# Performance work log

Hardware: AMD Instinct MI355X
Metric: run time of the kernel (lower is better)

Reference implementation:

```python
import jax, jax.numpy as jnp
import numpy as np

V, E, H2, B, T, OUT = 50000, 300, 512, 32, 512, 256
H = H2 // 2  # hidden per direction


def _rand_mask(key, lengths, n_true):
    # exactly n_true True positions per row, all within the valid prefix [0, len)
    t = jnp.arange(T)[None, :]
    r = jax.random.uniform(key, (B, T)) + (t >= lengths[:, None]) * 10.0
    idx = jnp.argsort(r, axis=1)[:, :n_true]
    mask = jnp.zeros((B, T), dtype=bool)
    return mask.at[jnp.arange(B)[:, None], idx].set(True)


def setup_inputs() -> dict:
    key = jax.random.key(0)
    ks = jax.random.split(key, 12)
    inputs = jax.random.randint(ks[0], (B, T), 0, V)
    lengths = jnp.sort(jax.random.randint(ks[1], (B,), OUT, T + 1))[::-1]
    lengths = lengths.at[0].set(T)  # max length == padded length
    fmask = _rand_mask(ks[2], lengths, OUT)
    bmask = _rand_mask(ks[3], lengths, OUT)
    emb_scale = np.sqrt(3.0 / E).astype(np.float32)
    emb = jax.random.uniform(ks[4], (V, E), minval=-emb_scale, maxval=emb_scale, dtype=jnp.float32)
    k = 1.0 / np.sqrt(H).astype(np.float32)
    def u(kk, shape):
        return jax.random.uniform(kk, shape, minval=-k, maxval=k, dtype=jnp.float32)
    return {
        'inputs': inputs, 'seq_length': lengths, 'fmask': fmask, 'bmask': bmask,
        'out_seq_length': OUT, 'emb': emb,
        'W_ih_f': u(ks[5], (4 * H, E)), 'W_hh_f': u(ks[6], (4 * H, H)),
        'b_ih_f': u(ks[7], (4 * H,)), 'b_hh_f': u(ks[8], (4 * H,)),
        'W_ih_b': u(ks[9], (4 * H, E)), 'W_hh_b': u(ks[10], (4 * H, H)),
        'b_ih_b': u(ks[11], (4 * H,)), 'b_hh_b': u(ks[7], (4 * H,)),
    }


def run_lstm(xe, W_ih, W_hh, b_ih, b_hh):
    # PyTorch LSTM cell, gate order i,f,g,o. xe: (B,T,E) -> (B,T,H)
    xg = jnp.einsum('bte,ge->btg', xe, W_ih) + (b_ih + b_hh)
    def step(carry, xg_t):
        h, c = carry
        g = xg_t + h @ W_hh.T
        i, f, gg, o = jnp.split(g, 4, axis=-1)
        c = jax.nn.sigmoid(f) * c + jax.nn.sigmoid(i) * jnp.tanh(gg)
        h = jax.nn.sigmoid(o) * jnp.tanh(c)
        return (h, c), h
    h0 = jnp.zeros((xe.shape[0], W_hh.shape[1]), xe.dtype)
    _, hs = jax.lax.scan(step, (h0, h0), xg.transpose(1, 0, 2))
    return hs.transpose(1, 0, 2)


def select_masked(x, mask, out_len):
    # masked_select row-major order == indices of True in increasing t
    idx = jnp.argsort(jnp.logical_not(mask), axis=1, stable=True)[:, :out_len]
    return jnp.take_along_axis(x, idx[:, :, None], axis=1)


def reference(inputs, seq_length, fmask, bmask, out_seq_length, emb,
              W_ih_f, W_hh_f, b_ih_f, b_hh_f, W_ih_b, W_hh_b, b_ih_b, b_hh_b):
    t = jnp.arange(inputs.shape[1])[None, :]          # (1,T)
    valid = t < seq_length[:, None]                   # (B,T)
    # forward direction (dropout is identity at inference)
    f_out = run_lstm(emb[inputs], W_ih_f, W_hh_f, b_ih_f, b_hh_f)
    f_out = f_out * valid[..., None]                  # pad_packed zeros beyond len
    fsel = select_masked(f_out, fmask, out_seq_length)
    # per-batch sequence reversal of valid prefix (padding stays in place)
    rev_idx = jnp.where(valid, seq_length[:, None] - 1 - t, t)
    rinputs = jnp.take_along_axis(inputs, rev_idx, axis=1)
    b_out = run_lstm(emb[rinputs], W_ih_b, W_hh_b, b_ih_b, b_hh_b)
    b_out = b_out * valid[..., None]
    bsel = select_masked(b_out, bmask, out_seq_length)
    # re-reverse selected backward outputs per batch
    k = jnp.minimum(seq_length, out_seq_length)[:, None]
    t2 = jnp.arange(out_seq_length)[None, :]
    idx2 = jnp.where(t2 < k, out_seq_length - 1 - t2, t2 - k)
    bsel = jnp.take_along_axis(bsel, idx2[:, :, None], axis=1)
    return jnp.concatenate([fsel, bsel], axis=2)      # (B,out_seq,2H)
```

## Files before the change

kernel.cpp:

```cpp
#include <hip/hip_runtime.h>
#include <hip/hip_bf16.h>

#define B_   32
#define T_   512
#define E_   300
#define H_   256
#define OUT_ 256
#define ECH  100
#define GROWP 293

typedef unsigned long long u64;

__global__ __launch_bounds__(64) void slots_kernel(
    const unsigned char* __restrict__ fm, const unsigned char* __restrict__ bm,
    int* __restrict__ fslot, int* __restrict__ bpos)
{
    __shared__ unsigned char fL[B_ * T_];
    __shared__ unsigned char bL[B_ * T_];
    const int tid = threadIdx.x;

    const unsigned int* fw = (const unsigned int*)fm;
    int cnt = 0;
    for (int i = tid; i < 128; i += 64) {
        unsigned int v = fw[i];
        cnt += ((v & 0xFFu) != 0) + ((v & 0xFF00u) != 0)
             + ((v & 0xFF0000u) != 0) + ((v >> 24) != 0);
    }
#pragma unroll
    for (int off = 32; off; off >>= 1) cnt += __shfl_down(cnt, off, 64);
    bool isbool = __shfl(cnt, 0, 64) > 128;

    if (isbool) {
        for (int i = tid; i < B_ * T_ / 4; i += 64) {
            ((unsigned int*)fL)[i] = ((const unsigned int*)fm)[i];
            ((unsigned int*)bL)[i] = ((const unsigned int*)bm)[i];
        }
    } else {
        const unsigned int* bw = (const unsigned int*)bm;
        for (int i = tid; i < B_ * T_; i += 64) {
            fL[i] = fw[i] != 0;
            bL[i] = bw[i] != 0;
        }
    }
    __syncthreads();

    if (tid < B_) {
        int jf = 0, jb = 0;
        for (int t = 0; t < T_; ++t) {
            bool f = fL[tid * T_ + t] != 0;
            bool g = bL[tid * T_ + t] != 0;
            fslot[tid * T_ + t] = f ? (jf++) : -1;
            bpos [tid * T_ + t] = g ? (OUT_ - 1 - (jb++)) : -1;
        }
    }
}

__global__ __launch_bounds__(256) void xg_gemm(
    const int* __restrict__ inputs, const int* __restrict__ seqlen,
    const float* __restrict__ emb,
    const float* __restrict__ Wihf, const float* __restrict__ Wihb,
    const float* __restrict__ bihf, const float* __restrict__ bhhf,
    const float* __restrict__ bihb, const float* __restrict__ bhhb,
    float* __restrict__ xg, int t0, int TcMax)
{
    const int tg   = blockIdx.y;
    const int dir  = blockIdx.z;
    const int rblk = blockIdx.x * 64;
    const int tid  = threadIdx.x;

    __shared__ float eL[4][B_][ECH];
    __shared__ int   tokS[4][B_];

    if (tid < 128) {
        int t4 = tid >> 5, b = tid & 31;
        int t = t0 + tg * 4 + t4;
        int L = seqlen[b];
        int tt = t;
        if (dir) tt = (t < L) ? (L - 1 - t) : t;
        tokS[t4][b] = inputs[b * T_ + tt];
    }

    const float* W = dir ? Wihb : Wihf;
    const int b  = tid & 31;
    const int r8 = tid >> 5;

    float acc[4][8];
#pragma unroll
    for (int t4 = 0; t4 < 4; ++t4)
#pragma unroll
        for (int m = 0; m < 8; ++m) acc[t4][m] = 0.f;

    for (int ec = 0; ec < 3; ++ec) {
        __syncthreads();
        for (int idx = tid; idx < 3200; idx += 256) {
            int q  = idx % 25;
            int bb = (idx / 25) & 31;
            int t4 = idx / (25 * 32);
            const float* erow = emb + (size_t)tokS[t4][bb] * E_ + ec * ECH;
            *(float4*)&eL[t4][bb][q * 4] = *(const float4*)(erow + q * 4);
        }
        __syncthreads();

        for (int e4 = 0; e4 < 25; ++e4) {
            float4 w4[8];
#pragma unroll
            for (int m = 0; m < 8; ++m)
                w4[m] = *(const float4*)(W + (size_t)(rblk + r8 + m * 8) * E_
                                         + ec * ECH + e4 * 4);
#pragma unroll
            for (int t4 = 0; t4 < 4; ++t4) {
                float4 h4 = *(const float4*)&eL[t4][b][e4 * 4];
#pragma unroll
                for (int m = 0; m < 8; ++m)
                    acc[t4][m] += h4.x * w4[m].x + h4.y * w4[m].y
                                + h4.z * w4[m].z + h4.w * w4[m].w;
            }
        }
    }

    const float* bi = dir ? bihb : bihf;
    const float* bh = dir ? bhhb : bhhf;
#pragma unroll
    for (int t4 = 0; t4 < 4; ++t4) {
        float* outp = xg + (size_t)(dir * TcMax + tg * 4 + t4) * (1024 * B_);
#pragma unroll
        for (int m = 0; m < 8; ++m) {
            int row = rblk + r8 + m * 8;
            outp[(size_t)row * B_ + b] = acc[t4][m] + bi[row] + bh[row];
        }
    }
}

__global__ __launch_bounds__(512, 2) void persist_rec(
    const float* __restrict__ xg, const int* __restrict__ seqlen,
    const float* __restrict__ Whh_f, const float* __restrict__ Whh_b,
    const int* __restrict__ fslot, const int* __restrict__ bpos,
    float* __restrict__ hbuf, float* __restrict__ cbuf,
    int* __restrict__ barr, float* __restrict__ out, int t0, int Tc)
{
    const int wg  = blockIdx.x;
    const int dir = wg >> 6;
    const int wgd = wg & 63;
    const int u0  = wgd * 4;
    const int tid = threadIdx.x;

    const int rg  = tid & 3;
    const int bgr = (tid >> 2) & 7;
    const int kq  = tid >> 5;

    __shared__ float hP[128 * 68];
    __shared__ float gbuf[16 * GROWP];
    __shared__ int   sL[B_];

    const float* Whh = dir ? Whh_b : Whh_f;
    float w[4][16];
#pragma unroll
    for (int r = 0; r < 4; ++r) {
        const float* wr = Whh + (size_t)(rg * H_ + u0 + r) * H_ + kq * 16;
#pragma unroll
        for (int q = 0; q < 4; ++q) {
            float4 v = *(const float4*)(wr + q * 4);
            w[r][q * 4 + 0] = v.x; w[r][q * 4 + 1] = v.y;
            w[r][q * 4 + 2] = v.z; w[r][q * 4 + 3] = v.w;
        }
    }
    if (tid < B_) sL[tid] = seqlen[tid];
    __syncthreads();

    const int ul = (tid >> 5) & 3, bb = tid & 31;
    float c_reg = 0.f;
    if (t0 > 0 && tid < 128)
        c_reg = cbuf[(size_t)(dir * 64 + wgd) * 128 + ul * 32 + bb];

    float xgv0 = 0.f, xgv1 = 0.f, xgv2 = 0.f, xgv3 = 0.f;
    if (tid < 128) {
        const float* xp = xg + (size_t)(dir * Tc) * 32768 + (u0 + ul) * 32 + bb;
        xgv0 = xp[0];
        xgv1 = xp[256 * 32];
        xgv2 = xp[512 * 32];
        xgv3 = xp[768 * 32];
    }

    int* myflag = barr + dir * 64 + wgd;

    for (int tc = 0; tc < Tc; ++tc) {
        const int t = t0 + tc;

        float xgn0 = 0.f, xgn1 = 0.f, xgn2 = 0.f, xgn3 = 0.f;
        if (tc + 1 < Tc && tid < 128) {
            const float* xp = xg + (size_t)(dir * Tc + tc + 1) * 32768 + (u0 + ul) * 32 + bb;
            xgn0 = xp[0];
            xgn1 = xp[256 * 32];
            xgn2 = xp[512 * 32];
            xgn3 = xp[768 * 32];
        }

        if (tc > 0) {
            if (tid < 64) {
                const int* fp = barr + dir * 64 + tid;
                while (!__all(__hip_atomic_load(fp, __ATOMIC_RELAXED,
                                                __HIP_MEMORY_SCOPE_AGENT) >= tc))
                    __builtin_amdgcn_s_sleep(1);
            }
            __syncthreads();
        }

        u64 hr[8];
        if (t > 0) {
            const u64* hp64 = (const u64*)(hbuf +
                (size_t)(dir * 2 + ((t - 1) & 1)) * (64 * 32 * 4));
#pragma unroll
            for (int i = 0; i < 8; ++i)
                hr[i] = __hip_atomic_load(hp64 + tid + 512 * i, __ATOMIC_RELAXED,
                                          __HIP_MEMORY_SCOPE_AGENT);
#pragma unroll
            for (int i = 0; i < 8; ++i) {
                int g = tid + 512 * i;
                int f4 = g >> 1, jp = g & 1;
                int k4 = f4 >> 5, b = f4 & 31;
                int base = ((k4 >> 2) * 8 + (b >> 2)) * 68 + (k4 & 3) * 16 + (b & 3);
                union { u64 u; float f[2]; } cv; cv.u = hr[i];
                hP[base + 8 * jp]     = cv.f[0];
                hP[base + 8 * jp + 4] = cv.f[1];
            }
        }
        __syncthreads();

        float acc[4][4];
#pragma unroll
        for (int r = 0; r < 4; ++r)
#pragma unroll
            for (int bi = 0; bi < 4; ++bi) acc[r][bi] = 0.f;

        if (t > 0) {
            const float* hblk = &hP[(kq * 8 + bgr) * 68];
#pragma unroll
            for (int kk = 0; kk < 16; ++kk) {
                float4 h4 = *(const float4*)(hblk + kk * 4);
#pragma unroll
                for (int r = 0; r < 4; ++r) {
                    acc[r][0] += w[r][kk] * h4.x;
                    acc[r][1] += w[r][kk] * h4.y;
                    acc[r][2] += w[r][kk] * h4.z;
                    acc[r][3] += w[r][kk] * h4.w;
                }
            }
        }

#pragma unroll
        for (int r = 0; r < 4; ++r)
#pragma unroll
            for (int bi = 0; bi < 4; ++bi)
                acc[r][bi] += __shfl_xor(acc[r][bi], 32, 64);

        if (((tid >> 5) & 1) == 0) {
            const int kq2 = kq >> 1;
#pragma unroll
            for (int r = 0; r < 4; ++r)
#pragma unroll
                for (int bi = 0; bi < 4; ++bi)
                    gbuf[(r * 4 + rg) * GROWP + (bgr * 4 + bi) * 9 + kq2] = acc[r][bi];
        }
        __syncthreads();

        if (tid < 128) {
            const int u = u0 + ul;
            float hnew;
            if (t < sL[bb]) {
                float gi = xgv0, gf = xgv1, gg = xgv2, go = xgv3;
#pragma unroll
                for (int q = 0; q < 8; ++q) {
                    gi += gbuf[(ul * 4 + 0) * GROWP + bb * 9 + q];
                    gf += gbuf[(ul * 4 + 1) * GROWP + bb * 9 + q];
                    gg += gbuf[(ul * 4 + 2) * GROWP + bb * 9 + q];
                    go += gbuf[(ul * 4 + 3) * GROWP + bb * 9 + q];
                }
                float si = 1.f / (1.f + expf(-gi));
                float sf = 1.f / (1.f + expf(-gf));
                float so = 1.f / (1.f + expf(-go));
                c_reg = sf * c_reg + si * tanhf(gg);
                hnew  = so * tanhf(c_reg);
                if (dir == 0) {
                    int j = fslot[bb * T_ + t];
                    if (j >= 0)
                        __hip_atomic_store(&out[((size_t)bb * OUT_ + j) * 512 + u],
                                           hnew, __ATOMIC_RELAXED,
                                           __HIP_MEMORY_SCOPE_AGENT);
                } else {
                    int p = bpos[bb * T_ + t];
                    if (p >= 0)
                        __hip_atomic_store(&out[((size_t)bb * OUT_ + p) * 512 + 256 + u],
                                           hnew, __ATOMIC_RELAXED,
                                           __HIP_MEMORY_SCOPE_AGENT);
                }
            } else {
                hnew = hP[((u >> 4) * 8 + (bb >> 2)) * 68 + (u & 15) * 4 + (bb & 3)];
            }
            float* hn = hbuf + (size_t)(dir * 2 + (t & 1)) * (64 * 32 * 4);
            __hip_atomic_store(&hn[(wgd * 32 + bb) * 4 + ul], hnew,
                               __ATOMIC_RELAXED, __HIP_MEMORY_SCOPE_AGENT);
        }
        xgv0 = xgn0; xgv1 = xgn1; xgv2 = xgn2; xgv3 = xgn3;
        __syncthreads();

        if (tc + 1 < Tc && tid == 0)
            __hip_atomic_store(myflag, tc + 1, __ATOMIC_RELAXED,
                               __HIP_MEMORY_SCOPE_AGENT);
    }

    if (tid < 128)
        cbuf[(size_t)(dir * 64 + wgd) * 128 + ul * 32 + bb] = c_reg;
}

extern "C" void kernel_launch(void* const* d_in, const int* in_sizes, int n_in,
                              void* d_out, int out_size, void* d_ws, size_t ws_size,
                              hipStream_t stream) {
    const int*           inputs = (const int*)d_in[0];
    const int*           seqlen = (const int*)d_in[1];
    const unsigned char* fm     = (const unsigned char*)d_in[2];
    const unsigned char* bm     = (const unsigned char*)d_in[3];
    const float* emb  = (const float*)d_in[5];
    const float* Wihf = (const float*)d_in[6];
    const float* Whhf = (const float*)d_in[7];
    const float* bihf = (const float*)d_in[8];
    const float* bhhf = (const float*)d_in[9];
    const float* Wihb = (const float*)d_in[10];
    const float* Whhb = (const float*)d_in[11];
    const float* bihb = (const float*)d_in[12];
    const float* bhhb = (const float*)d_in[13];
    float* out = (float*)d_out;

    char* ws = (char*)d_ws;
    int*   fslot = (int*)(ws);
    int*   bpos  = (int*)(ws + 65536);
    float* hbuf  = (float*)(ws + 131072);
    float* cbuf  = (float*)(ws + 262144);
    int*   barr  = (int*)(ws + 327680);
    float* xg    = (float*)(ws + 393216);
    (void)in_sizes; (void)n_in; (void)out_size;

    size_t avail = (ws_size > 393216) ? ws_size - 393216 : 0;
    int Tc = 4;
    for (int c = 512; c >= 4; c >>= 1)
        if ((size_t)c * 262144 <= avail) { Tc = c; break; }

    slots_kernel<<<1, 64, 0, stream>>>(fm, bm, fslot, bpos);

    for (int t0 = 0; t0 < T_; t0 += Tc) {
        dim3 g(16, Tc / 4, 2);
        xg_gemm<<<g, 256, 0, stream>>>(inputs, seqlen, emb, Wihf, Wihb,
                                       bihf, bhhf, bihb, bhhb, xg, t0, Tc);
        hipMemsetAsync(barr, 0, 512, stream);
        persist_rec<<<128, 512, 0, stream>>>(xg, seqlen, Whhf, Whhb,
                                             fslot, bpos, hbuf, cbuf, barr, out, t0, Tc);
    }
}
```

Baseline: 2.324 ms.

## Fuse input-projection GEMM into persistent LSTM kernel with producer-consumer flags

Merges the input projection GEMM and the recurrent kernel into one launch of 256 workgroups. The extra 128 workgroups compute the projected gate inputs in 4-step groups and publish per-group completion counters, while the recurrent workgroups poll those counters before reading each group. This is meant to overlap the projection GEMM with the serial recurrence and remove a separate kernel launch. The cost is relying on co-residency of all 256 workgroups, extra polling on each step's barrier, and atomic loads and stores on the gate-input buffer.

New measurement: 2.087 ms. -10.2%, faster.

```diff
diff --git a/kernel.cpp b/kernel.cpp
--- a/kernel.cpp
+++ b/kernel.cpp
@@ -131,28 +131,117 @@
     }
 }
 
-__global__ __launch_bounds__(512, 2) void persist_rec(
-    const float* __restrict__ xg, const int* __restrict__ seqlen,
-    const float* __restrict__ Whh_f, const float* __restrict__ Whh_b,
+__global__ __launch_bounds__(512, 2) void fused_lstm(
+    const int* __restrict__ inputs, const int* __restrict__ seqlen,
+    const float* __restrict__ emb,
+    const float* __restrict__ Wihf, const float* __restrict__ Whhf,
+    const float* __restrict__ bihf, const float* __restrict__ bhhf,
+    const float* __restrict__ Wihb, const float* __restrict__ Whhb,
+    const float* __restrict__ bihb, const float* __restrict__ bhhb,
     const int* __restrict__ fslot, const int* __restrict__ bpos,
     float* __restrict__ hbuf, float* __restrict__ cbuf,
-    int* __restrict__ barr, float* __restrict__ out, int t0, int Tc)
+    int* __restrict__ barr, int* __restrict__ xgcnt,
+    float* __restrict__ xg, float* __restrict__ out,
+    int t0, int Tc, int fused)
 {
     const int wg  = blockIdx.x;
+    const int tid = threadIdx.x;
+    __shared__ __align__(16) float smem[13824];
+
+    if (wg >= 128) {
+        float* eL   = smem;
+        int*   tokS = (int*)(smem + 12800);
+        const int hw = wg - 128;
+
+        for (int j = hw; j < 2048; j += 128) {
+            const int tg  = j >> 4;
+            const int dir = (j >> 3) & 1;
+            const int rp  = j & 7;
+            const int rblk = (rp * 2 + (tid >> 8)) * 64;
+
+            if (tid < 128) {
+                int t4 = tid >> 5, b = tid & 31;
+                int t = tg * 4 + t4;
+                int L = seqlen[b];
+                int tt = t;
+                if (dir) tt = (t < L) ? (L - 1 - t) : t;
+                tokS[t4 * B_ + b] = inputs[b * T_ + tt];
+            }
+
+            const float* W  = dir ? Wihb : Wihf;
+            const int ltid = tid & 255;
+            const int b  = ltid & 31;
+            const int r8 = ltid >> 5;
+
+            float acc[4][8];
+#pragma unroll
+            for (int t4 = 0; t4 < 4; ++t4)
+#pragma unroll
+                for (int m = 0; m < 8; ++m) acc[t4][m] = 0.f;
+
+            for (int ec = 0; ec < 3; ++ec) {
+                __syncthreads();
+                for (int idx = tid; idx < 3200; idx += 512) {
+                    int q  = idx % 25;
+                    int bb = (idx / 25) & 31;
+                    int t4 = idx / (25 * 32);
+                    const float* erow = emb + (size_t)tokS[t4 * B_ + bb] * E_ + ec * ECH;
+                    *(float4*)&eL[(t4 * B_ + bb) * ECH + q * 4] = *(const float4*)(erow + q * 4);
+                }
+                __syncthreads();
+
+                for (int e4 = 0; e4 < 25; ++e4) {
+                    float4 w4[8];
+#pragma unroll
+                    for (int m = 0; m < 8; ++m)
+                        w4[m] = *(const float4*)(W + (size_t)(rblk + r8 + m * 8) * E_
+                                                 + ec * ECH + e4 * 4);
+#pragma unroll
+                    for (int t4 = 0; t4 < 4; ++t4) {
+                        float4 h4 = *(const float4*)&eL[(t4 * B_ + b) * ECH + e4 * 4];
+#pragma unroll
+                        for (int m = 0; m < 8; ++m)
+                            acc[t4][m] += h4.x * w4[m].x + h4.y * w4[m].y
+                                        + h4.z * w4[m].z + h4.w * w4[m].w;
+                    }
+                }
+            }
+
+            const float* bi = dir ? bihb : bihf;
+            const float* bh = dir ? bhhb : bhhf;
+#pragma unroll
+            for (int t4 = 0; t4 < 4; ++t4) {
+                float* outp = xg + (size_t)(dir * 512 + tg * 4 + t4) * (1024 * B_);
+#pragma unroll
+                for (int m = 0; m < 8; ++m) {
+                    int row = rblk + r8 + m * 8;
+                    __hip_atomic_store(&outp[(size_t)row * B_ + b],
+                                       acc[t4][m] + bi[row] + bh[row],
+                                       __ATOMIC_RELAXED, __HIP_MEMORY_SCOPE_AGENT);
+                }
+            }
+            __syncthreads();
+            if (tid == 0)
+                __hip_atomic_fetch_add(&xgcnt[dir * 128 + tg], 1,
+                                       __ATOMIC_RELAXED, __HIP_MEMORY_SCOPE_AGENT);
+        }
+        return;
+    }
+
+    float* hP   = smem;
+    float* gbuf = smem + 8704;
+    int*   sL   = (int*)(smem + 8704 + 4688);
+
     const int dir = wg >> 6;
     const int wgd = wg & 63;
     const int u0  = wgd * 4;
-    const int tid = threadIdx.x;
 
     const int rg  = tid & 3;
     const int bgr = (tid >> 2) & 7;
     const int kq  = tid >> 5;
 
-    __shared__ float hP[128 * 68];
-    __shared__ float gbuf[16 * GROWP];
-    __shared__ int   sL[B_];
-
-    const float* Whh = dir ? Whh_b : Whh_f;
+    const float* Whh = dir ? Whhb : Whhf;
+
     float w[4][16];
 #pragma unroll
     for (int r = 0; r < 4; ++r) {
@@ -172,37 +261,54 @@
     if (t0 > 0 && tid < 128)
         c_reg = cbuf[(size_t)(dir * 64 + wgd) * 128 + ul * 32 + bb];
 
+    if (fused) {
+        if (tid == 0) {
+            const int* xc = xgcnt + dir * 128 + (t0 >> 2);
+            while (__hip_atomic_load(xc, __ATOMIC_RELAXED,
+                                     __HIP_MEMORY_SCOPE_AGENT) < 8)
+                __builtin_amdgcn_s_sleep(1);
+        }
+        __syncthreads();
+    }
     float xgv0 = 0.f, xgv1 = 0.f, xgv2 = 0.f, xgv3 = 0.f;
     if (tid < 128) {
         const float* xp = xg + (size_t)(dir * Tc) * 32768 + (u0 + ul) * 32 + bb;
-        xgv0 = xp[0];
-        xgv1 = xp[256 * 32];
-        xgv2 = xp[512 * 32];
-        xgv3 = xp[768 * 32];
+        xgv0 = __hip_atomic_load(xp, __ATOMIC_RELAXED, __HIP_MEMORY_SCOPE_AGENT);
+        xgv1 = __hip_atomic_load(xp + 256 * 32, __ATOMIC_RELAXED, __HIP_MEMORY_SCOPE_AGENT);
+        xgv2 = __hip_atomic_load(xp + 512 * 32, __ATOMIC_RELAXED, __HIP_MEMORY_SCOPE_AGENT);
+        xgv3 = __hip_atomic_load(xp + 768 * 32, __ATOMIC_RELAXED, __HIP_MEMORY_SCOPE_AGENT);
     }
 
     int* myflag = barr + dir * 64 + wgd;
 
     for (int tc = 0; tc < Tc; ++tc) {
         const int t = t0 + tc;
+
+        if (tc > 0) {
+            if (tid < 64) {
+                const int* fp = barr + dir * 64 + tid;
+                const int gneed = (fused && tc + 1 < Tc) ? ((t0 + tc + 1) >> 2) : -1;
+                const int* xc = xgcnt + dir * 128 + (gneed < 0 ? 0 : gneed);
+                for (;;) {
+                    bool ok = __hip_atomic_load(fp, __ATOMIC_RELAXED,
+                                                __HIP_MEMORY_SCOPE_AGENT) >= tc;
+                    if (gneed >= 0 && tid == 0)
+                        ok = ok && (__hip_atomic_load(xc, __ATOMIC_RELAXED,
+                                                      __HIP_MEMORY_SCOPE_AGENT) >= 8);
+                    if (__all(ok)) break;
+                    __builtin_amdgcn_s_sleep(1);
+                }
+            }
+            __syncthreads();
+        }
 
         float xgn0 = 0.f, xgn1 = 0.f, xgn2 = 0.f, xgn3 = 0.f;
         if (tc + 1 < Tc && tid < 128) {
             const float* xp = xg + (size_t)(dir * Tc + tc + 1) * 32768 + (u0 + ul) * 32 + bb;
-            xgn0 = xp[0];
-            xgn1 = xp[256 * 32];
-            xgn2 = xp[512 * 32];
-            xgn3 = xp[768 * 32];
-        }
-
-        if (tc > 0) {
-            if (tid < 64) {
-                const int* fp = barr + dir * 64 + tid;
-                while (!__all(__hip_atomic_load(fp, __ATOMIC_RELAXED,
-                                                __HIP_MEMORY_SCOPE_AGENT) >= tc))
-                    __builtin_amdgcn_s_sleep(1);
-            }
-            __syncthreads();
+            xgn0 = __hip_atomic_load(xp, __ATOMIC_RELAXED, __HIP_MEMORY_SCOPE_AGENT);
+            xgn1 = __hip_atomic_load(xp + 256 * 32, __ATOMIC_RELAXED, __HIP_MEMORY_SCOPE_AGENT);
+            xgn2 = __hip_atomic_load(xp + 512 * 32, __ATOMIC_RELAXED, __HIP_MEMORY_SCOPE_AGENT);
+            xgn3 = __hip_atomic_load(xp + 768 * 32, __ATOMIC_RELAXED, __HIP_MEMORY_SCOPE_AGENT);
         }
 
         u64 hr[8];
@@ -336,6 +442,7 @@
     float* hbuf  = (float*)(ws + 131072);
     float* cbuf  = (float*)(ws + 262144);
     int*   barr  = (int*)(ws + 327680);
+    int*   xgcnt = (int*)(ws + 328192);
     float* xg    = (float*)(ws + 393216);
     (void)in_sizes; (void)n_in; (void)out_size;
 
@@ -346,12 +453,22 @@
 
     slots_kernel<<<1, 64, 0, stream>>>(fm, bm, fslot, bpos);
 
-    for (int t0 = 0; t0 < T_; t0 += Tc) {
-        dim3 g(16, Tc / 4, 2);
-        xg_gemm<<<g, 256, 0, stream>>>(inputs, seqlen, emb, Wihf, Wihb,
-                                       bihf, bhhf, bihb, bhhb, xg, t0, Tc);
-        hipMemsetAsync(barr, 0, 512, stream);
-        persist_rec<<<128, 512, 0, stream>>>(xg, seqlen, Whhf, Whhb,
-                                             fslot, bpos, hbuf, cbuf, barr, out, t0, Tc);
+    if (Tc == 512) {
+        (void)hipMemsetAsync(barr, 0, 512 + 1024, stream);
+        fused_lstm<<<256, 512, 0, stream>>>(
+            inputs, seqlen, emb, Wihf, Whhf, bihf, bhhf,
+            Wihb, Whhb, bihb, bhhb, fslot, bpos,
+            hbuf, cbuf, barr, xgcnt, xg, out, 0, 512, 1);
+    } else {
+        for (int t0 = 0; t0 < T_; t0 += Tc) {
+            dim3 g(16, Tc / 4, 2);
+            xg_gemm<<<g, 256, 0, stream>>>(inputs, seqlen, emb, Wihf, Wihb,
+                                           bihf, bhhf, bihb, bhhb, xg, t0, Tc);
+            (void)hipMemsetAsync(barr, 0, 512 + 1024, stream);
+            fused_lstm<<<128, 512, 0, stream>>>(
+                inputs, seqlen, emb, Wihf, Whhf, bihf, bhhf,
+                Wihb, Whhb, bihb, bhhb, fslot, bpos,
+                hbuf, cbuf, barr, xgcnt, xg, out, t0, Tc, 0);
+        }
     }
 }
```
